# Optimization experiments

Hardware: AMD Instinct MI355X
Metric: run time of the kernel (lower is better)

The kernel has to match this reference:

```python
import jax, jax.numpy as jnp
import numpy as np

N_HEADS = 8
D_EMBED = 512
D_HEAD = D_EMBED // N_HEADS
BS, SEQ = 2, 4096


def setup_inputs() -> dict:
    key = jax.random.key(0)
    ks = jax.random.split(key, 9)
    s = 1.0 / np.sqrt(D_EMBED)
    inp = {
        "x": jax.random.normal(ks[0], (BS, SEQ, D_EMBED), dtype=jnp.float32),
        "wq": jax.random.uniform(ks[1], (D_EMBED, D_EMBED), jnp.float32, -s, s),
        "bq": jax.random.uniform(ks[2], (D_EMBED,), jnp.float32, -s, s),
        "wk": jax.random.uniform(ks[3], (D_EMBED, D_EMBED), jnp.float32, -s, s),
        "bk": jax.random.uniform(ks[4], (D_EMBED,), jnp.float32, -s, s),
        "wv": jax.random.uniform(ks[5], (D_EMBED, D_EMBED), jnp.float32, -s, s),
        "bv": jax.random.uniform(ks[6], (D_EMBED,), jnp.float32, -s, s),
        "wo": jax.random.uniform(ks[7], (D_EMBED, D_EMBED), jnp.float32, -s, s),
        "bo": jax.random.uniform(ks[8], (D_EMBED,), jnp.float32, -s, s),
        "causal_mask": 1,
    }
    return inp


def reference(x, wq, bq, wk, bk, wv, bv, wo, bo, causal_mask):
    bs, seq, d = x.shape
    # torch Linear: y = x @ W^T + b, then SiLU gate
    q = jax.nn.silu(jnp.einsum('bsd,ed->bse', x, wq) + bq)
    k = jax.nn.silu(jnp.einsum('bsd,ed->bse', x, wk) + bk)
    v = jax.nn.silu(jnp.einsum('bsd,ed->bse', x, wv) + bv)
    # split heads: [b, h, s, dh]
    q = q.reshape(bs, seq, N_HEADS, D_HEAD).transpose(0, 2, 1, 3)
    k = k.reshape(bs, seq, N_HEADS, D_HEAD).transpose(0, 2, 1, 3)
    v = v.reshape(bs, seq, N_HEADS, D_HEAD).transpose(0, 2, 1, 3)
    scores = jnp.einsum('bhqd,bhkd->bhqk', q, k)  # [b,h,s,s]
    if causal_mask:
        mask = jnp.triu(jnp.ones((seq, seq), dtype=bool), k=1)
        scores = jnp.where(mask, -jnp.inf, scores)
    scores = scores / jnp.sqrt(jnp.asarray(D_HEAD, dtype=scores.dtype))
    attn = jax.nn.softmax(scores, axis=-1)
    out = jnp.einsum('bhqk,bhkd->bhqd', attn, v)
    out = out.transpose(0, 2, 1, 3).reshape(bs, seq, d)
    return jnp.einsum('bsd,ed->bse', out, wo) + bo
```

## Files before the change

kernel.cpp:

```cpp
#include <hip/hip_runtime.h>
#include <stdint.h>


typedef float  f32x4  __attribute__((ext_vector_type(4)));
typedef float  f32x16 __attribute__((ext_vector_type(16)));
typedef short  bf16x8 __attribute__((ext_vector_type(8)));
typedef unsigned int u32x4 __attribute__((ext_vector_type(4)));

#define DEV static __device__ __forceinline__

#define BSZ   2
#define SEQL  4096
#define NHEAD 8
#define DHEAD 64
#define DEMB  512
#define MROWS (BSZ*SEQL)
#define NXE   (MROWS*DEMB)
#define NWE   (DEMB*DEMB)

DEV void async_copy16(const void* g, void* l) {
  __builtin_amdgcn_global_load_lds(
      (const __attribute__((address_space(1))) void*)g,
      (__attribute__((address_space(3))) void*)l,
      16, 0, 0);
}

DEV unsigned short f2bf_bits(float f) {
  unsigned int x = __float_as_uint(f);
  x = x + 0x7FFFu + ((x >> 16) & 1u);
  return (unsigned short)(x >> 16);
}

__global__ __launch_bounds__(256) void convert_all(
    const float* __restrict__ x,
    const float* __restrict__ wq, const float* __restrict__ wk,
    const float* __restrict__ wv, const float* __restrict__ wo,
    unsigned short* __restrict__ dst)
{
  const int nch = (NXE + 4 * NWE) / 4;
  for (int c = blockIdx.x * 256 + threadIdx.x; c < nch; c += gridDim.x * 256) {
    const int off = c * 4;
    const float* src;
    int rel;
    if (off < NXE) {
      src = x; rel = off;
    } else {
      int rr = off - NXE;
      int j = rr >> 18;
      rel = rr & (NWE - 1);
      src = (j == 0) ? wq : (j == 1) ? wk : (j == 2) ? wv : wo;
    }
    float4 v = *(const float4*)(src + rel);
    ushort4 o = make_ushort4(f2bf_bits(v.x), f2bf_bits(v.y),
                             f2bf_bits(v.z), f2bf_bits(v.w));
    *(ushort4*)(dst + off) = o;
  }
}

DEV void gemm_mainloop(const unsigned short* __restrict__ A,
                       const unsigned short* __restrict__ B,
                       int arow0, int brow0,
                       unsigned short* Ash, unsigned short* Bsh,
                       int t, f32x4 acc[4][4])
{
  const int l = t & 63;
  const int w = t >> 6, wr = w >> 1, wc = w & 1;
  for (int kt = 0; kt < 8; ++kt) {
    const int k0 = kt * 64;
#pragma unroll
    for (int i = 0; i < 4; ++i) {
      int p = t + i * 256;
      int r = p >> 3;
      int c0 = ((p & 7) ^ (r & 7)) * 8;
      async_copy16(A + (size_t)(arow0 + r) * DEMB + k0 + c0, (char*)Ash + p * 16);
      async_copy16(B + (size_t)(brow0 + r) * DEMB + k0 + c0, (char*)Bsh + p * 16);
    }
    __syncthreads();

    bf16x8 af[4][2], bf[4][2];
#pragma unroll
    for (int m = 0; m < 4; ++m)
#pragma unroll
      for (int ks = 0; ks < 2; ++ks) {
        int r = wr * 64 + m * 16 + (l & 15);
        int c = (ks * 4 + (l >> 4)) ^ (r & 7);
        af[m][ks] = *(const bf16x8*)((const char*)Ash + r * 128 + c * 16);
      }
#pragma unroll
    for (int n = 0; n < 4; ++n)
#pragma unroll
      for (int ks = 0; ks < 2; ++ks) {
        int r = wc * 64 + n * 16 + (l & 15);
        int c = (ks * 4 + (l >> 4)) ^ (r & 7);
        bf[n][ks] = *(const bf16x8*)((const char*)Bsh + r * 128 + c * 16);
      }
#pragma unroll
    for (int m = 0; m < 4; ++m)
#pragma unroll
      for (int n = 0; n < 4; ++n)
#pragma unroll
        for (int ks = 0; ks < 2; ++ks)
          acc[m][n] = __builtin_amdgcn_mfma_f32_16x16x32_bf16(
              af[m][ks], bf[n][ks], acc[m][n], 0, 0, 0);
    __syncthreads();
  }
}

__global__ __launch_bounds__(256) void qkv_gemm(
    const unsigned short* __restrict__ xb,
    const unsigned short* __restrict__ wqb,
    const unsigned short* __restrict__ wkb,
    const unsigned short* __restrict__ wvb,
    const float* __restrict__ bq, const float* __restrict__ bk,
    const float* __restrict__ bv,
    unsigned short* __restrict__ q_out,
    unsigned short* __restrict__ k_out,
    unsigned short* __restrict__ v_out)
{
  __shared__ unsigned short Ash[128 * 64];
  __shared__ unsigned short Bsh[128 * 64];
  const int z = blockIdx.z;
  const unsigned short* W = (z == 0) ? wqb : (z == 1) ? wkb : wvb;
  const float* bias = (z == 0) ? bq : (z == 1) ? bk : bv;
  unsigned short* dst = (z == 0) ? q_out : (z == 1) ? k_out : v_out;

  f32x4 acc[4][4];
#pragma unroll
  for (int m = 0; m < 4; ++m)
#pragma unroll
    for (int n = 0; n < 4; ++n) acc[m][n] = (f32x4){0.f, 0.f, 0.f, 0.f};

  gemm_mainloop(xb, W, blockIdx.x * 128, blockIdx.y * 128, Ash, Bsh,
                threadIdx.x, acc);

  const int t = threadIdx.x, l = t & 63, w = t >> 6, wr = w >> 1, wc = w & 1;
  const float qscale = (z == 0) ? 0.18033688011112042f : 1.0f;
#pragma unroll
  for (int n = 0; n < 4; ++n) {
    const int e = blockIdx.y * 128 + wc * 64 + n * 16 + (l & 15);
    const float bval = bias[e];
    const int h = e >> 6, d = e & 63;
#pragma unroll
    for (int m = 0; m < 4; ++m)
#pragma unroll
      for (int g = 0; g < 4; ++g) {
        const int R = blockIdx.x * 128 + wr * 64 + m * 16 + (l >> 4) * 4 + g;
        float v = acc[m][n][g] + bval;
        v = v / (1.0f + __expf(-v));
        v *= qscale;
        const int b = R >> 12, s = R & 4095;
        const int head = b * NHEAD + h;
        size_t off;
        if (z == 1) {
          const int kt = s >> 5, ql = s & 31;
          const int dt = d >> 4, hi = (d >> 3) & 1, ee = d & 7;
          const int lane = (hi << 5) | ql;
          off = (size_t)head * (SEQL * DHEAD) +
                (size_t)(((kt << 2) + dt) << 9) + (lane << 3) + ee;
        } else {
          off = (((size_t)head) * SEQL + s) * DHEAD + d;
        }
        dst[off] = f2bf_bits(v);
      }
  }
}

__global__ __launch_bounds__(256) void vtrans(
    const unsigned short* __restrict__ vb, unsigned short* __restrict__ vtb)
{
  __shared__ unsigned short tile[64 * 66];
  const int t = threadIdx.x;
  const int bh = blockIdx.y;
  const int s0 = blockIdx.x * 64;
#pragma unroll
  for (int i = 0; i < 2; ++i) {
    int p = t + i * 256;
    int r = p >> 3, c0 = (p & 7) * 8;
    bf16x8 v = *(const bf16x8*)(vb + ((size_t)bh * SEQL + s0 + r) * DHEAD + c0);
#pragma unroll
    for (int j = 0; j < 8; ++j) tile[r * 66 + c0 + j] = (unsigned short)v[j];
  }
  __syncthreads();
#pragma unroll
  for (int i = 0; i < 2; ++i) {
    int p = t + i * 256;
    int dh = p >> 3, c0 = (p & 7) * 8;
    bf16x8 o;
#pragma unroll
    for (int j = 0; j < 8; ++j) o[j] = (short)tile[(c0 + j) * 66 + dh];
    const int sb = s0 + c0;
    const int kt = sb >> 5, rem = sb & 31;
    const int hf = rem >> 4, hi = (rem >> 3) & 1;
    const int n = dh >> 5, ql = dh & 31;
    const int lane = (hi << 5) | ql;
    const size_t off = (size_t)bh * (SEQL * DHEAD) +
        (size_t)((((kt << 1) + n) << 1) + hf) * 512 + (lane << 3);
    *(bf16x8*)(vtb + off) = o;
  }
}

__global__ __launch_bounds__(256) void attn_fwd(
    const unsigned short* __restrict__ qb,
    const unsigned short* __restrict__ kfb,
    const unsigned short* __restrict__ vfb,
    unsigned short* __restrict__ attnb,
    const int* __restrict__ causal_ptr)
{
  __shared__ float Osh[2][32][65];
  __shared__ float Lsh[2][32];

  const int t = threadIdx.x;
  const int l = t & 63;
  const int ql = l & 31;
  const int hi = l >> 5;
  const int wid = t >> 6;
  const int r = wid & 1;
  const int h = wid >> 1;
  const int bid = blockIdx.x;
  const int cc = bid & 255, qq = bid >> 8;
  const int g = cc >> 4;
  const int head = cc & 15;
  const int j = (qq == 0) ? (63 - g) : (qq == 1) ? g
              : (qq == 2) ? (47 - g) : (16 + g);
  const int q0w = j * 64 + r * 32;
  const int causal = causal_ptr[0];

  const unsigned short* qbase = qb + (size_t)head * SEQL * DHEAD;
  const unsigned short* kbase = kfb + (size_t)head * SEQL * DHEAD;
  const unsigned short* vbase = vfb + (size_t)head * SEQL * DHEAD;

  bf16x8 qf[4];
#pragma unroll
  for (int dt = 0; dt < 4; ++dt)
    qf[dt] = *(const bf16x8*)(qbase +
        (unsigned)((q0w + ql) * DHEAD + dt * 16 + hi * 8));

  f32x16 o0, o1;
#pragma unroll
  for (int i = 0; i < 16; ++i) { o0[i] = 0.f; o1[i] = 0.f; }
  float rl = 0.f;

  const int T = causal ? 2 * (j + 1) : (SEQL / 32);
  const int ktm = (T + 1) >> 1;
  const int kt0 = h ? ktm : 0;
  const int kt1 = h ? T : ktm;

  const unsigned l8 = (unsigned)(l << 3);

  for (int kt = kt0; kt < kt1; ++kt) {
    const int k0 = kt * 32;

    const unsigned short* kp = kbase + ((unsigned)(kt << 2) << 9) + l8;
    bf16x8 kf[4];
#pragma unroll
    for (int dt = 0; dt < 4; ++dt)
      kf[dt] = *(const bf16x8*)(kp + (dt << 9));

    const unsigned short* vp = vbase + ((unsigned)(kt << 2) << 9) + l8;
    bf16x8 vf[2][2];
#pragma unroll
    for (int n = 0; n < 2; ++n)
#pragma unroll
      for (int hf = 0; hf < 2; ++hf)
        vf[n][hf] = *(const bf16x8*)(vp + (((n << 1) + hf) << 9));

    f32x16 s;
#pragma unroll
    for (int i = 0; i < 16; ++i) s[i] = 0.f;
#pragma unroll
    for (int dt = 0; dt < 4; ++dt)
      s = __builtin_amdgcn_mfma_f32_32x32x16_bf16(kf[dt], qf[dt], s, 0, 0, 0);

    if (causal && (k0 + 31 > q0w)) {
      const int qrow = q0w + ql;
#pragma unroll
      for (int rg = 0; rg < 16; ++rg) {
        const int kk = k0 + (rg & 3) + 8 * (rg >> 2) + 4 * hi;
        s[rg] = (kk > qrow) ? -1e30f : s[rg];
      }
    }

#pragma unroll
    for (int rg = 0; rg < 16; ++rg)
      s[rg] = __builtin_amdgcn_exp2f(s[rg]);

    rl += (((s[0] + s[1]) + (s[2] + s[3])) + ((s[4] + s[5]) + (s[6] + s[7])))
        + (((s[8] + s[9]) + (s[10] + s[11])) + ((s[12] + s[13]) + (s[14] + s[15])));

#pragma unroll
    for (int hf = 0; hf < 2; ++hf) {
      const int b8 = hf * 8;
      float e0 = s[b8 + 0], e1 = s[b8 + 1], e2 = s[b8 + 2], e3 = s[b8 + 3];
      float e4 = s[b8 + 4], e5 = s[b8 + 5], e6 = s[b8 + 6], e7 = s[b8 + 7];
      unsigned a0, a1, b0, b1;
      asm("v_cvt_pk_bf16_f32 %0, %1, %2" : "=v"(a0) : "v"(e0), "v"(e1));
      asm("v_cvt_pk_bf16_f32 %0, %1, %2" : "=v"(a1) : "v"(e2), "v"(e3));
      asm("v_cvt_pk_bf16_f32 %0, %1, %2" : "=v"(b0) : "v"(e4), "v"(e5));
      asm("v_cvt_pk_bf16_f32 %0, %1, %2" : "=v"(b1) : "v"(e6), "v"(e7));
      asm("v_permlane32_swap_b32 %0, %1" : "+v"(a0), "+v"(b0));
      asm("v_permlane32_swap_b32 %0, %1" : "+v"(a1), "+v"(b1));
      u32x4 pau = {a0, a1, b0, b1};
      bf16x8 pa = *(bf16x8*)&pau;
      o0 = __builtin_amdgcn_mfma_f32_32x32x16_bf16(pa, vf[0][hf], o0, 0, 0, 0);
      o1 = __builtin_amdgcn_mfma_f32_32x32x16_bf16(pa, vf[1][hf], o1, 0, 0, 0);
    }
  }

  rl += __shfl_xor(rl, 32);

  if (h == 1) {
#pragma unroll
    for (int rg = 0; rg < 16; ++rg) {
      const int cr = (rg & 3) + 8 * (rg >> 2) + 4 * hi;
      Osh[r][cr][ql] = o0[rg];
      Osh[r][cr][32 + ql] = o1[rg];
    }
    if (l < 32) Lsh[r][l] = rl;
  }
  __syncthreads();
  if (h == 0) {
    const float inv = 1.0f / (rl + Lsh[r][ql]);
    const int b2 = head >> 3, hh = head & 7;
#pragma unroll
    for (int rg = 0; rg < 16; ++rg) {
      const int cr = (rg & 3) + 8 * (rg >> 2) + 4 * hi;
      const float invr = __shfl(inv, cr);
      const int srow = q0w + cr;
      const float v0 = (o0[rg] + Osh[r][cr][ql]) * invr;
      const float v1 = (o1[rg] + Osh[r][cr][32 + ql]) * invr;
      unsigned short* dst = attnb + ((size_t)b2 * SEQL + srow) * DEMB + hh * DHEAD;
      dst[ql] = f2bf_bits(v0);
      dst[32 + ql] = f2bf_bits(v1);
    }
  }
}

__global__ __launch_bounds__(256) void out_gemm(
    const unsigned short* __restrict__ ab,
    const unsigned short* __restrict__ wob,
    const float* __restrict__ bo,
    float* __restrict__ out)
{
  __shared__ unsigned short Ash[128 * 64];
  __shared__ unsigned short Bsh[128 * 64];
  f32x4 acc[4][4];
#pragma unroll
  for (int m = 0; m < 4; ++m)
#pragma unroll
    for (int n = 0; n < 4; ++n) acc[m][n] = (f32x4){0.f, 0.f, 0.f, 0.f};

  gemm_mainloop(ab, wob, blockIdx.x * 128, blockIdx.y * 128, Ash, Bsh,
                threadIdx.x, acc);

  const int t = threadIdx.x, l = t & 63, w = t >> 6, wr = w >> 1, wc = w & 1;
#pragma unroll
  for (int n = 0; n < 4; ++n) {
    const int e = blockIdx.y * 128 + wc * 64 + n * 16 + (l & 15);
    const float bval = bo[e];
#pragma unroll
    for (int m = 0; m < 4; ++m)
#pragma unroll
      for (int g = 0; g < 4; ++g) {
        const int R = blockIdx.x * 128 + wr * 64 + m * 16 + (l >> 4) * 4 + g;
        out[(size_t)R * DEMB + e] = acc[m][n][g] + bval;
      }
  }
}

extern "C" void kernel_launch(void* const* d_in, const int* in_sizes, int n_in,
                              void* d_out, int out_size, void* d_ws, size_t ws_size,
                              hipStream_t stream)
{
  const float* x  = (const float*)d_in[0];
  const float* wq = (const float*)d_in[1];
  const float* bq = (const float*)d_in[2];
  const float* wk = (const float*)d_in[3];
  const float* bk = (const float*)d_in[4];
  const float* wv = (const float*)d_in[5];
  const float* bv = (const float*)d_in[6];
  const float* wo = (const float*)d_in[7];
  const float* bo = (const float*)d_in[8];
  const int* causal = (const int*)d_in[9];
  float* out = (float*)d_out;

  unsigned short* ws  = (unsigned short*)d_ws;
  unsigned short* xb  = ws;
  unsigned short* wqb = xb + NXE;
  unsigned short* wkb = wqb + NWE;
  unsigned short* wvb = wkb + NWE;
  unsigned short* wob = wvb + NWE;
  unsigned short* qb  = wob + NWE;
  unsigned short* kfb = qb + NXE;
  unsigned short* vb2 = kfb + NXE;
  unsigned short* vfb = vb2 + NXE;
  unsigned short* atb = vfb + NXE;

  convert_all<<<dim3(1024), dim3(256), 0, stream>>>(x, wq, wk, wv, wo, xb);
  qkv_gemm<<<dim3(64, 4, 3), dim3(256), 0, stream>>>(
      xb, wqb, wkb, wvb, bq, bk, bv, qb, kfb, vb2);
  vtrans<<<dim3(64, 16), dim3(256), 0, stream>>>(vb2, vfb);
  attn_fwd<<<dim3(1024), dim3(256), 0, stream>>>(qb, kfb, vfb, atb, causal);
  out_gemm<<<dim3(64, 4, 1), dim3(256), 0, stream>>>(atb, wob, bo, out);
}
```

Measured before the change: 102.8 us.

## Fuse V transpose into QKV epilogue and balance causal attention work across warps

```diff
diff --git a/kernel.cpp b/kernel.cpp
--- a/kernel.cpp
+++ b/kernel.cpp
@@ -157,6 +157,12 @@
           const int lane = (hi << 5) | ql;
           off = (size_t)head * (SEQL * DHEAD) +
                 (size_t)(((kt << 2) + dt) << 9) + (lane << 3) + ee;
+        } else if (z == 2) {
+          const int kt = s >> 5, hf = (s >> 4) & 1, hi = (s >> 3) & 1, ee = s & 7;
+          const int nn = d >> 5, ql = d & 31;
+          const int lane = (hi << 5) | ql;
+          off = (size_t)head * (SEQL * DHEAD) +
+                (size_t)((((kt << 1) + nn) << 1) + hf) * 512 + (lane << 3) + ee;
         } else {
           off = (((size_t)head) * SEQL + s) * DHEAD + d;
         }
@@ -165,69 +171,19 @@
   }
 }
 
-__global__ __launch_bounds__(256) void vtrans(
-    const unsigned short* __restrict__ vb, unsigned short* __restrict__ vtb)
-{
-  __shared__ unsigned short tile[64 * 66];
-  const int t = threadIdx.x;
-  const int bh = blockIdx.y;
-  const int s0 = blockIdx.x * 64;
-#pragma unroll
-  for (int i = 0; i < 2; ++i) {
-    int p = t + i * 256;
-    int r = p >> 3, c0 = (p & 7) * 8;
-    bf16x8 v = *(const bf16x8*)(vb + ((size_t)bh * SEQL + s0 + r) * DHEAD + c0);
-#pragma unroll
-    for (int j = 0; j < 8; ++j) tile[r * 66 + c0 + j] = (unsigned short)v[j];
-  }
-  __syncthreads();
-#pragma unroll
-  for (int i = 0; i < 2; ++i) {
-    int p = t + i * 256;
-    int dh = p >> 3, c0 = (p & 7) * 8;
-    bf16x8 o;
-#pragma unroll
-    for (int j = 0; j < 8; ++j) o[j] = (short)tile[(c0 + j) * 66 + dh];
-    const int sb = s0 + c0;
-    const int kt = sb >> 5, rem = sb & 31;
-    const int hf = rem >> 4, hi = (rem >> 3) & 1;
-    const int n = dh >> 5, ql = dh & 31;
-    const int lane = (hi << 5) | ql;
-    const size_t off = (size_t)bh * (SEQL * DHEAD) +
-        (size_t)((((kt << 1) + n) << 1) + hf) * 512 + (lane << 3);
-    *(bf16x8*)(vtb + off) = o;
-  }
-}
-
-__global__ __launch_bounds__(256) void attn_fwd(
-    const unsigned short* __restrict__ qb,
-    const unsigned short* __restrict__ kfb,
-    const unsigned short* __restrict__ vfb,
-    unsigned short* __restrict__ attnb,
-    const int* __restrict__ causal_ptr)
-{
-  __shared__ float Osh[2][32][65];
-  __shared__ float Lsh[2][32];
-
-  const int t = threadIdx.x;
-  const int l = t & 63;
-  const int ql = l & 31;
-  const int hi = l >> 5;
-  const int wid = t >> 6;
-  const int r = wid & 1;
-  const int h = wid >> 1;
-  const int bid = blockIdx.x;
-  const int cc = bid & 255, qq = bid >> 8;
-  const int g = cc >> 4;
-  const int head = cc & 15;
-  const int j = (qq == 0) ? (63 - g) : (qq == 1) ? g
-              : (qq == 2) ? (47 - g) : (16 + g);
-  const int q0w = j * 64 + r * 32;
-  const int causal = causal_ptr[0];
-
+DEV void run_range(const unsigned short* __restrict__ qb,
+                   const unsigned short* __restrict__ kfb,
+                   const unsigned short* __restrict__ vfb,
+                   int head, int jslab, int r, int kta, int ktb, int causal,
+                   int ql, int hi, int l,
+                   float* __restrict__ OaccS,
+                   float* __restrict__ LaccS)
+{
+  const int q0w = jslab * 64 + r * 32;
   const unsigned short* qbase = qb + (size_t)head * SEQL * DHEAD;
   const unsigned short* kbase = kfb + (size_t)head * SEQL * DHEAD;
   const unsigned short* vbase = vfb + (size_t)head * SEQL * DHEAD;
+  const unsigned l8 = (unsigned)(l << 3);
 
   bf16x8 qf[4];
 #pragma unroll
@@ -240,14 +196,7 @@
   for (int i = 0; i < 16; ++i) { o0[i] = 0.f; o1[i] = 0.f; }
   float rl = 0.f;
 
-  const int T = causal ? 2 * (j + 1) : (SEQL / 32);
-  const int ktm = (T + 1) >> 1;
-  const int kt0 = h ? ktm : 0;
-  const int kt1 = h ? T : ktm;
-
-  const unsigned l8 = (unsigned)(l << 3);
-
-  for (int kt = kt0; kt < kt1; ++kt) {
+  for (int kt = kta; kt < ktb; ++kt) {
     const int k0 = kt * 32;
 
     const unsigned short* kp = kbase + ((unsigned)(kt << 2) << 9) + l8;
@@ -307,31 +256,84 @@
   }
 
   rl += __shfl_xor(rl, 32);
-
-  if (h == 1) {
-#pragma unroll
-    for (int rg = 0; rg < 16; ++rg) {
-      const int cr = (rg & 3) + 8 * (rg >> 2) + 4 * hi;
-      Osh[r][cr][ql] = o0[rg];
-      Osh[r][cr][32 + ql] = o1[rg];
+#pragma unroll
+  for (int rg = 0; rg < 16; ++rg) {
+    const int cr = (rg & 3) + 8 * (rg >> 2) + 4 * hi;
+    atomicAdd(&OaccS[cr * 64 + ql], o0[rg]);
+    atomicAdd(&OaccS[cr * 64 + 32 + ql], o1[rg]);
+  }
+  if (hi == 0) atomicAdd(&LaccS[ql], rl);
+}
+
+__global__ __launch_bounds__(256) void attn_fwd(
+    const unsigned short* __restrict__ qb,
+    const unsigned short* __restrict__ kfb,
+    const unsigned short* __restrict__ vfb,
+    unsigned short* __restrict__ attnb,
+    const int* __restrict__ causal_ptr)
+{
+  __shared__ float Oacc[2][32][64];
+  __shared__ float Lacc[2][32];
+
+  const int t = threadIdx.x;
+  const int l = t & 63;
+  const int ql = l & 31;
+  const int hi = l >> 5;
+  const int e = t >> 6;
+  const int bid = blockIdx.x;
+  const int head = bid & 15;
+  const int p = (bid >> 4) & 31;
+  const int r = bid >> 9;
+  const int jH = 63 - p, jL = p;
+  const int causal = causal_ptr[0];
+
+  {
+    float* z = (float*)Oacc;
+    for (int i = t; i < 2 * 32 * 64; i += 256) z[i] = 0.f;
+    if (t < 64) ((float*)Lacc)[t] = 0.f;
+  }
+  __syncthreads();
+
+  const int TrH = causal ? (2 * jH + r + 1) : 128;
+  const int TrL = causal ? (2 * jL + r + 1) : 128;
+  const int W = TrH + TrL;
+  const int i0 = (W * e) >> 2;
+  const int i1 = (W * (e + 1)) >> 2;
+
+  {
+    const int h0 = (i0 < TrH) ? i0 : TrH;
+    const int h1 = (i1 < TrH) ? i1 : TrH;
+    if (h0 < h1)
+      run_range(qb, kfb, vfb, head, jH, r, h0, h1, causal, ql, hi, l,
+                &Oacc[0][0][0], &Lacc[0][0]);
+  }
+  {
+    const int l0 = (i0 > TrH) ? (i0 - TrH) : 0;
+    const int l1 = (i1 > TrH) ? (i1 - TrH) : 0;
+    if (l0 < l1)
+      run_range(qb, kfb, vfb, head, jL, r, l0, l1, causal, ql, hi, l,
+                &Oacc[1][0][0], &Lacc[1][0]);
+  }
+  __syncthreads();
+
+  {
+    const int s = t >> 7;
+    const int rem = t & 127;
+    const int row = rem >> 2;
+    const int c0 = (rem & 3) * 16;
+    const int js = s ? jL : jH;
+    const int srow = js * 64 + r * 32 + row;
+    const float inv = 1.0f / Lacc[s][row];
+    const int b2 = head >> 3, hh = head & 7;
+    bf16x8 oA, oB;
+#pragma unroll
+    for (int jj = 0; jj < 8; ++jj) {
+      oA[jj] = (short)f2bf_bits(Oacc[s][row][c0 + jj] * inv);
+      oB[jj] = (short)f2bf_bits(Oacc[s][row][c0 + 8 + jj] * inv);
     }
-    if (l < 32) Lsh[r][l] = rl;
-  }
-  __syncthreads();
-  if (h == 0) {
-    const float inv = 1.0f / (rl + Lsh[r][ql]);
-    const int b2 = head >> 3, hh = head & 7;
-#pragma unroll
-    for (int rg = 0; rg < 16; ++rg) {
-      const int cr = (rg & 3) + 8 * (rg >> 2) + 4 * hi;
-      const float invr = __shfl(inv, cr);
-      const int srow = q0w + cr;
-      const float v0 = (o0[rg] + Osh[r][cr][ql]) * invr;
-      const float v1 = (o1[rg] + Osh[r][cr][32 + ql]) * invr;
-      unsigned short* dst = attnb + ((size_t)b2 * SEQL + srow) * DEMB + hh * DHEAD;
-      dst[ql] = f2bf_bits(v0);
-      dst[32 + ql] = f2bf_bits(v1);
-    }
+    unsigned short* dst = attnb + ((size_t)b2 * SEQL + srow) * DEMB + hh * DHEAD + c0;
+    *(bf16x8*)dst = oA;
+    *(bf16x8*)(dst + 8) = oB;
   }
 }
 
@@ -391,14 +393,12 @@
   unsigned short* wob = wvb + NWE;
   unsigned short* qb  = wob + NWE;
   unsigned short* kfb = qb + NXE;
-  unsigned short* vb2 = kfb + NXE;
-  unsigned short* vfb = vb2 + NXE;
+  unsigned short* vfb = kfb + NXE;
   unsigned short* atb = vfb + NXE;
 
   convert_all<<<dim3(1024), dim3(256), 0, stream>>>(x, wq, wk, wv, wo, xb);
   qkv_gemm<<<dim3(64, 4, 3), dim3(256), 0, stream>>>(
-      xb, wqb, wkb, wvb, bq, bk, bv, qb, kfb, vb2);
-  vtrans<<<dim3(64, 16), dim3(256), 0, stream>>>(vb2, vfb);
+      xb, wqb, wkb, wvb, bq, bk, bv, qb, kfb, vfb);
   attn_fwd<<<dim3(1024), dim3(256), 0, stream>>>(qb, kfb, vfb, atb, causal);
   out_gemm<<<dim3(64, 4, 1), dim3(256), 0, stream>>>(atb, wob, bo, out);
 }
```

New measurement: 151.2 us. 1.47x slower.
